# Optimization experiments

Measured on AMD Instinct MI355X. Metric: run time of the kernel, lower is better.

The kernel has to match this reference:

```python
import jax, jax.numpy as jnp
import numpy as np

B, S, D_IN = 2, 2048, 1024
H = 16
HD = 64  # head_dim = d_out // head_cnt


def setup_inputs() -> dict:
    key = jax.random.key(0)
    kx, kq, kk, kv = jax.random.split(key, 4)
    x = jax.random.normal(kx, (B, S, D_IN), dtype=jnp.float32)
    # Per-head Q/K/V projection weights, stacked: [H, d_in, head_dim].
    # Matches nn.Linear(d_in, head_out) per head (qkv_bias=False), scaled like
    # a typical init.
    sc = 1.0 / np.sqrt(D_IN)
    Wq = jax.random.normal(kq, (H, D_IN, HD), dtype=jnp.float32) * sc
    Wk = jax.random.normal(kk, (H, D_IN, HD), dtype=jnp.float32) * sc
    Wv = jax.random.normal(kv, (H, D_IN, HD), dtype=jnp.float32) * sc
    return {"x": x, "Wq": Wq, "Wk": Wk, "Wv": Wv}


def reference(x, Wq, Wk, Wv):
    # Batched multi-head causal attention equivalent to the per-head loop +
    # torch.cat(dim=-1): head h's output occupies slice [h*HD:(h+1)*HD].
    q = jnp.einsum("bsd,hde->bhse", x, Wq)  # [B,H,S,HD]
    k = jnp.einsum("bsd,hde->bhse", x, Wk)
    v = jnp.einsum("bsd,hde->bhse", x, Wv)
    scale = 1.0 / jnp.sqrt(jnp.asarray(HD, dtype=x.dtype))
    scores = jnp.einsum("bhse,bhte->bhst", q, k) * scale  # [B,H,S,S]
    seq = x.shape[1]
    causal = jnp.tril(jnp.ones((seq, seq), dtype=bool))
    scores = jnp.where(causal, scores, jnp.asarray(-jnp.inf, dtype=scores.dtype))
    attn = jax.nn.softmax(scores, axis=-1)  # dropout = 0.0 -> identity
    ctx = jnp.einsum("bhst,bhte->bhse", attn, v)  # [B,H,S,HD]
    # concat heads on last dim
    b, h, s, e = ctx.shape
    return ctx.transpose(0, 2, 1, 3).reshape(b, s, h * e)
```

## Files before the change

### kernel.cpp

```cpp
#include <hip/hip_runtime.h>


#define DI   1024
#define HD   64
#define NH   16
#define SEQ  2048
#define NB   2

typedef unsigned short u16;
typedef unsigned short us8 __attribute__((ext_vector_type(8)));
typedef unsigned short us4 __attribute__((ext_vector_type(4)));
typedef unsigned int   u32x2 __attribute__((ext_vector_type(2)));
typedef short bf8 __attribute__((ext_vector_type(8)));
typedef float f4 __attribute__((ext_vector_type(4)));

#define MFMA16(a, b, c) __builtin_amdgcn_mfma_f32_16x16x32_bf16((a), (b), (c), 0, 0, 0)

#if __has_builtin(__builtin_amdgcn_exp2f)
#define EXP2(x) __builtin_amdgcn_exp2f(x)
#else
#define EXP2(x) exp2f(x)
#endif

#if __has_builtin(__builtin_amdgcn_perm)
#define PKHI(a, b) __builtin_amdgcn_perm((a), (b), 0x07060302u)
#else
__device__ __forceinline__ unsigned PKHI(unsigned a, unsigned b) {
  return (b >> 16) | (a & 0xffff0000u);
}
#endif

__device__ __forceinline__ u16 f2bf(float f) {
  unsigned u = __float_as_uint(f);
  u += 0x7fffu + ((u >> 16) & 1u);
  return (u16)(u >> 16);
}

__device__ __forceinline__ void async16(const u16* g, u16* l) {
  __builtin_amdgcn_global_load_lds((const __attribute__((address_space(1))) void*)g,
                                   (__attribute__((address_space(3))) void*)l,
                                   16, 0, 0);
}

__global__ __launch_bounds__(256) void prep_k(const float* __restrict__ x,
                                              const float* __restrict__ Wq,
                                              const float* __restrict__ Wk,
                                              const float* __restrict__ Wv,
                                              u16* __restrict__ xb,
                                              u16* __restrict__ Wt) {
  __shared__ __align__(16) u16 tile[64][72];
  const int bid = blockIdx.x;
  if (bid < 2048) {
    const int i = (bid * 256 + threadIdx.x) * 8;
    float4 v0 = *(const float4*)(x + i);
    float4 v1 = *(const float4*)(x + i + 4);
    us8 o;
    o[0] = f2bf(v0.x); o[1] = f2bf(v0.y); o[2] = f2bf(v0.z); o[3] = f2bf(v0.w);
    o[4] = f2bf(v1.x); o[5] = f2bf(v1.y); o[6] = f2bf(v1.z); o[7] = f2bf(v1.w);
    *(us8*)(xb + i) = o;
    return;
  }
  const int idx = bid - 2048;
  const int mh = idx >> 4;
  const int d0 = (idx & 15) * 64;
  const int mat = mh >> 4, h = mh & 15;
  const float* W = (mat == 0 ? Wq : (mat == 1 ? Wk : Wv)) + (size_t)h * DI * HD;
  const int t = threadIdx.x;
  {
    const int r = t >> 2, c = (t & 3) * 16;
    const float* src = W + (size_t)(d0 + r) * HD + c;
    #pragma unroll
    for (int j = 0; j < 4; j++) {
      float4 v = *(const float4*)(src + j * 4);
      tile[r][c + j * 4 + 0] = f2bf(v.x);
      tile[r][c + j * 4 + 1] = f2bf(v.y);
      tile[r][c + j * 4 + 2] = f2bf(v.z);
      tile[r][c + j * 4 + 3] = f2bf(v.w);
    }
  }
  __syncthreads();
  {
    const int e = t >> 2, c = (t & 3) * 16;
    __align__(16) u16 tmp[16];
    #pragma unroll
    for (int i = 0; i < 16; i++) tmp[i] = tile[c + i][e];
    u16* dst = Wt + ((size_t)mh * HD + e) * DI + d0 + c;
    *(us8*)dst       = *(us8*)&tmp[0];
    *(us8*)(dst + 8) = *(us8*)&tmp[8];
  }
}

__global__ __launch_bounds__(256, 2) void proj_k(const u16* __restrict__ x,
                                                 const u16* __restrict__ Wt,
                                                 u16* __restrict__ Qo,
                                                 u16* __restrict__ Ko,
                                                 u16* __restrict__ Vo) {
  __shared__ __align__(16) u16 smem[40960];
  u16* const xs = smem;
  u16* const ws = smem + 16384;
  const int m0 = blockIdx.x * 128, n0 = blockIdx.y * 192;
  const int tid = threadIdx.x, w = tid >> 6, lane = tid & 63;
  const int l15 = lane & 15, quad = lane >> 4, l7 = l15 & 7;
  const int lrow = lane >> 3, lch = lane & 7;
  const int wm = w >> 1, wn = w & 1;

  f4 acc[4][6];
  #pragma unroll
  for (int i = 0; i < 4; i++)
    #pragma unroll
    for (int j = 0; j < 6; j++) {
      f4 z = {0.f, 0.f, 0.f, 0.f};
      acc[i][j] = z;
    }

  const u16* xg = x  + (size_t)(m0 + lrow) * DI + ((lch ^ lrow) * 8);
  const u16* wg = Wt + (size_t)(n0 + lrow) * DI + ((lch ^ lrow) * 8);

  #pragma unroll
  for (int i = 0; i < 4; i++)
    async16(xg + (size_t)(i * 32 + w * 8) * DI, &xs[(i * 32 + w * 8) * 64]);
  #pragma unroll
  for (int c = 0; c < 6; c++)
    async16(wg + (size_t)(w * 48 + c * 8) * DI, &ws[(w * 48 + c * 8) * 64]);

  for (int it = 0; it < 16; it++) {
    const int cbx = (it & 1) * 8192, cbw = (it & 1) * 12288;
    __syncthreads();
    if (it + 1 < 16) {
      const int k1 = (it + 1) * 64;
      const int nbx = 8192 - cbx, nbw = 12288 - cbw;
      #pragma unroll
      for (int i = 0; i < 4; i++)
        async16(xg + (size_t)(i * 32 + w * 8) * DI + k1,
                &xs[nbx + (i * 32 + w * 8) * 64]);
      #pragma unroll
      for (int c = 0; c < 6; c++)
        async16(wg + (size_t)(w * 48 + c * 8) * DI + k1,
                &ws[nbw + (w * 48 + c * 8) * 64]);
    }
    #pragma unroll
    for (int ks = 0; ks < 64; ks += 32) {
      const int c0 = (ks >> 3) + quad;
      bf8 af[4], bfr[6];
      #pragma unroll
      for (int i = 0; i < 4; i++)
        af[i] = *(const bf8*)&xs[cbx + (wm * 64 + i * 16 + l15) * 64 + ((c0 ^ l7) * 8)];
      #pragma unroll
      for (int i = 0; i < 6; i++)
        bfr[i] = *(const bf8*)&ws[cbw + (wn * 96 + i * 16 + l15) * 64 + ((c0 ^ l7) * 8)];
      #pragma unroll
      for (int mi = 0; mi < 4; mi++)
        #pragma unroll
        for (int ni = 0; ni < 6; ni++)
          acc[mi][ni] = MFMA16(af[mi], bfr[ni], acc[mi][ni]);
    }
  }

  const float qscale = 0.125f * 1.44269504088896340736f;
  #pragma unroll
  for (int mi = 0; mi < 4; mi++) {
    const int mrow = m0 + wm * 64 + mi * 16 + quad * 4;
    const int b = mrow >> 11, sb = mrow & (SEQ - 1);
    #pragma unroll
    for (int ni = 0; ni < 6; ni++) {
      const int nf = n0 + wn * 96 + ni * 16;
      const int mat = nf >> 10;
      const int h = (nf >> 6) & 15;
      const int e = (nf & 63) + l15;
      if (mat == 2) {
        __align__(8) u16 pk[4];
        #pragma unroll
        for (int r = 0; r < 4; r++) pk[r] = f2bf(acc[mi][ni][r]);
        *(us4*)(Vo + (((size_t)b * NH + h) * HD + e) * SEQ + sb) = *(us4*)pk;
      } else {
        u16* O = mat ? Ko : Qo;
        const float sc = mat ? 1.0f : qscale;
        #pragma unroll
        for (int r = 0; r < 4; r++)
          O[(((size_t)b * NH + h) * SEQ + sb + r) * HD + e] = f2bf(acc[mi][ni][r] * sc);
      }
    }
  }
}

__global__ __launch_bounds__(256, 2) void attn_k(const u16* __restrict__ Qo,
                                                 const u16* __restrict__ Ko,
                                                 const u16* __restrict__ Vo,
                                                 float* __restrict__ out) {
  __shared__ __align__(16) u16 Ks[2 * 128 * 64];
  __shared__ __align__(16) u16 Vs[2 * 64 * 128];
  __shared__ __align__(16) u16 Ps[4 * 16 * 128];
  const int ia = blockIdx.x;
  const int ib = 31 - ia;
  const int bh = blockIdx.y;
  const int b = bh >> 4, h = bh & 15;
  const int tid = threadIdx.x, w = tid >> 6, lane = tid & 63;
  const int l15 = lane & 15, quad = lane >> 4;
  const int qh = quad >> 1, ql = quad & 1;

  const u16* Qb = Qo + (size_t)bh * SEQ * HD;
  const u16* Kb = Ko + (size_t)bh * SEQ * HD;
  const u16* Vb = Vo + (size_t)bh * HD * SEQ;

  const int qrowA = ia * 64 + w * 16 + l15;
  const int qrowB = ib * 64 + w * 16 + l15;
  bf8 bqA0 = *(const bf8*)(Qb + (size_t)qrowA * HD + quad * 8);
  bf8 bqA1 = *(const bf8*)(Qb + (size_t)qrowA * HD + 32 + quad * 8);
  bf8 bqB0 = *(const bf8*)(Qb + (size_t)qrowB * HD + quad * 8);
  bf8 bqB1 = *(const bf8*)(Qb + (size_t)qrowB * HD + 32 + quad * 8);

  f4 oA[4], oB[4], lA, lB;
  #pragma unroll
  for (int i = 0; i < 4; i++) {
    f4 z = {0.f, 0.f, 0.f, 0.f};
    oA[i] = z; oB[i] = z;
  }
  {
    f4 z = {0.f, 0.f, 0.f, 0.f};
    lA = z; lB = z;
  }
  const bf8 ones = {0x3F80, 0x3F80, 0x3F80, 0x3F80, 0x3F80, 0x3F80, 0x3F80, 0x3F80};

  const int nA = ia / 2 + 1, nB = ib / 2 + 1;

  const u16* ksp0 = &Ks[l15 * 64 + ((quad ^ (l15 & 7)) * 8)];
  const u16* ksp1 = &Ks[l15 * 64 + (((quad + 4) ^ (l15 & 7)) * 8)];
  const u16* vsp[4];
  #pragma unroll
  for (int tc = 0; tc < 4; tc++)
    vsp[tc] = &Vs[l15 * 128 + (((tc * 4 + quad) ^ l15) * 8)];
  u16* const psw = &Ps[w * 2048 + l15 * 128 + ql * 4];
  const u16* prp[4];
  #pragma unroll
  for (int tc = 0; tc < 4; tc++)
    prp[tc] = &Ps[w * 2048 + l15 * 128 + (((tc * 4 + quad) ^ l15) * 8)];

  const int kl = lane >> 3, kc = lane & 7;
  const int vl = lane >> 4, vc = lane & 15;
  const u16* kg = Kb + (size_t)(w * 32 + kl) * HD + ((kc ^ kl) * 8);
  const u16* vg[4];
  u16* ldsK[4];
  u16* ldsV[4];
  #pragma unroll
  for (int i = 0; i < 4; i++) {
    const int vr = w * 16 + i * 4;
    const int f = (i * 4 + vl) & 15;
    vg[i] = Vb + (size_t)(vr + vl) * SEQ + ((vc ^ f) * 8);
    ldsK[i] = &Ks[(w * 32 + i * 8) * 64];
    ldsV[i] = &Vs[vr * 128];
  }

  const int mqA = qrowA - (nA - 1) * 128 - quad * 4;
  const int mqB = qrowB - (nB - 1) * 128 - quad * 4;

  auto pphase = [&](f4* s, bool domask, int mq) {
    #pragma unroll
    for (int mf = 0; mf < 8; mf++) {
      f4 sv = s[mf];
      if (domask) {
        #pragma unroll
        for (int r = 0; r < 4; r++)
          sv[r] = (mf * 16 + r <= mq) ? sv[r] : -1e30f;
      }
      const unsigned p0 = __float_as_uint(EXP2(sv[0]));
      const unsigned p1 = __float_as_uint(EXP2(sv[1]));
      const unsigned p2 = __float_as_uint(EXP2(sv[2]));
      const unsigned p3 = __float_as_uint(EXP2(sv[3]));
      u32x2 pk = {PKHI(p1, p0), PKHI(p3, p2)};
      *(u32x2*)(psw + ((((mf << 1) | qh) ^ l15) * 8)) = pk;
    }
  };

  #pragma unroll
  for (int i = 0; i < 4; i++) {
    async16(kg + i * 512, ldsK[i]);
    async16(vg[i], ldsV[i]);
  }
  kg += 128 * HD;
  #pragma unroll
  for (int i = 0; i < 4; i++) vg[i] += 128;

  for (int it = 0; it < nB; it++) {
    const int cb = (it & 1) * 8192;
    __syncthreads();
    if (it + 1 < nB) {
      const int nb = 8192 - cb;
      #pragma unroll
      for (int i = 0; i < 4; i++) {
        async16(kg + i * 512, ldsK[i] + nb);
        async16(vg[i], ldsV[i] + nb);
      }
      kg += 128 * HD;
      #pragma unroll
      for (int i = 0; i < 4; i++) vg[i] += 128;
    }
    const bool doA = (it < nA);

    f4 sA[8], sB[8];
    #pragma unroll
    for (int mf = 0; mf < 8; mf++) {
      bf8 ak0 = *(const bf8*)(ksp0 + cb + mf * 1024);
      bf8 ak1 = *(const bf8*)(ksp1 + cb + mf * 1024);
      f4 z = {0.f, 0.f, 0.f, 0.f};
      f4 tb = MFMA16(ak0, bqB0, z);
      sB[mf] = MFMA16(ak1, bqB1, tb);
      if (doA) {
        f4 ta = MFMA16(ak0, bqA0, z);
        sA[mf] = MFMA16(ak1, bqA1, ta);
      }
    }

    pphase(sB, it == nB - 1, mqB);
    #pragma unroll
    for (int tc = 0; tc < 4; tc++) {
      bf8 pf = *(const bf8*)(prp[tc]);
      lB = MFMA16(ones, pf, lB);
      #pragma unroll
      for (int ef = 0; ef < 4; ef++) {
        bf8 vf = *(const bf8*)(vsp[tc] + cb + ef * 2048);
        oB[ef] = MFMA16(vf, pf, oB[ef]);
      }
    }
    if (doA) {
      pphase(sA, it == nA - 1, mqA);
      #pragma unroll
      for (int tc = 0; tc < 4; tc++) {
        bf8 pf = *(const bf8*)(prp[tc]);
        lA = MFMA16(ones, pf, lA);
        #pragma unroll
        for (int ef = 0; ef < 4; ef++) {
          bf8 vf = *(const bf8*)(vsp[tc] + cb + ef * 2048);
          oA[ef] = MFMA16(vf, pf, oA[ef]);
        }
      }
    }
  }

  const float invA = 1.0f / lA[0];
  const float invB = 1.0f / lB[0];
  float* opA = out + ((size_t)b * SEQ + qrowA) * (NH * HD) + h * HD + quad * 4;
  float* opB = out + ((size_t)b * SEQ + qrowB) * (NH * HD) + h * HD + quad * 4;
  #pragma unroll
  for (int ef = 0; ef < 4; ef++) {
    f4 va = oA[ef] * invA;
    f4 vb = oB[ef] * invB;
    *(float4*)(opA + ef * 16) = *(float4*)&va;
    *(float4*)(opB + ef * 16) = *(float4*)&vb;
  }
}

extern "C" void kernel_launch(void* const* d_in, const int* in_sizes, int n_in,
                              void* d_out, int out_size, void* d_ws, size_t ws_size,
                              hipStream_t stream) {
  const float* x  = (const float*)d_in[0];
  const float* Wq = (const float*)d_in[1];
  const float* Wk = (const float*)d_in[2];
  const float* Wv = (const float*)d_in[3];
  float* out = (float*)d_out;

  u16* xb = (u16*)d_ws;
  u16* Wt = xb + (size_t)NB * SEQ * DI;
  u16* Qo = Wt + (size_t)3 * NH * HD * DI;
  u16* Ko = Qo + (size_t)NB * NH * SEQ * HD;
  u16* Vo = Ko + (size_t)NB * NH * SEQ * HD;

  prep_k<<<dim3(2048 + 768), 256, 0, stream>>>(x, Wq, Wk, Wv, xb, Wt);
  proj_k<<<dim3(32, 16), 256, 0, stream>>>(xb, Wt, Qo, Ko, Vo);
  attn_k<<<dim3(16, 32), 256, 0, stream>>>(Qo, Ko, Vo, out);
}
```

Before: 147.1 us.

## Switch attention to 32x32 MFMA with register-resident P and one 128-row tile per block

Each block now processes a single 128-row query tile with 32x32x16 bf16 MFMAs instead of two paired 64-row tiles using 16x16 MFMAs. The softmax probabilities no longer go through LDS: they are packed and moved between lanes with v_permlane32_swap. The row sums are accumulated in VALU rather than with a ones-matrix MFMA. The work order is reversed for half of the batch-heads to balance causal work, and s_setprio is raised around the MFMA sections. This is meant to cut LDS traffic and MFMA instruction count, at the cost of more registers per thread and coarser load balancing across blocks.

```diff
diff --git a/kernel.cpp b/kernel.cpp
--- a/kernel.cpp
+++ b/kernel.cpp
@@ -13,8 +13,10 @@
 typedef unsigned int   u32x2 __attribute__((ext_vector_type(2)));
 typedef short bf8 __attribute__((ext_vector_type(8)));
 typedef float f4 __attribute__((ext_vector_type(4)));
+typedef float f16v __attribute__((ext_vector_type(16)));
 
 #define MFMA16(a, b, c) __builtin_amdgcn_mfma_f32_16x16x32_bf16((a), (b), (c), 0, 0, 0)
+#define MFMA32(a, b, c) __builtin_amdgcn_mfma_f32_32x32x16_bf16((a), (b), (c), 0, 0, 0)
 
 #if __has_builtin(__builtin_amdgcn_exp2f)
 #define EXP2(x) __builtin_amdgcn_exp2f(x)
@@ -189,51 +191,28 @@
                                                  float* __restrict__ out) {
   __shared__ __align__(16) u16 Ks[2 * 128 * 64];
   __shared__ __align__(16) u16 Vs[2 * 64 * 128];
-  __shared__ __align__(16) u16 Ps[4 * 16 * 128];
-  const int ia = blockIdx.x;
-  const int ib = 31 - ia;
-  const int bh = blockIdx.y;
+  __shared__ float Ls[128];
+  const int xt = blockIdx.x, bh = blockIdx.y;
+  const int t = (bh < 16) ? (15 - xt) : xt;
   const int b = bh >> 4, h = bh & 15;
   const int tid = threadIdx.x, w = tid >> 6, lane = tid & 63;
-  const int l15 = lane & 15, quad = lane >> 4;
-  const int qh = quad >> 1, ql = quad & 1;
+  const int l31 = lane & 31, hi = lane >> 5;
+  const int k7 = l31 & 7, v15 = l31 & 15;
+  const int nI = t + 1;
 
   const u16* Qb = Qo + (size_t)bh * SEQ * HD;
   const u16* Kb = Ko + (size_t)bh * SEQ * HD;
   const u16* Vb = Vo + (size_t)bh * HD * SEQ;
 
-  const int qrowA = ia * 64 + w * 16 + l15;
-  const int qrowB = ib * 64 + w * 16 + l15;
-  bf8 bqA0 = *(const bf8*)(Qb + (size_t)qrowA * HD + quad * 8);
-  bf8 bqA1 = *(const bf8*)(Qb + (size_t)qrowA * HD + 32 + quad * 8);
-  bf8 bqB0 = *(const bf8*)(Qb + (size_t)qrowB * HD + quad * 8);
-  bf8 bqB1 = *(const bf8*)(Qb + (size_t)qrowB * HD + 32 + quad * 8);
-
-  f4 oA[4], oB[4], lA, lB;
-  #pragma unroll
-  for (int i = 0; i < 4; i++) {
-    f4 z = {0.f, 0.f, 0.f, 0.f};
-    oA[i] = z; oB[i] = z;
-  }
-  {
-    f4 z = {0.f, 0.f, 0.f, 0.f};
-    lA = z; lB = z;
-  }
-  const bf8 ones = {0x3F80, 0x3F80, 0x3F80, 0x3F80, 0x3F80, 0x3F80, 0x3F80, 0x3F80};
-
-  const int nA = ia / 2 + 1, nB = ib / 2 + 1;
-
-  const u16* ksp0 = &Ks[l15 * 64 + ((quad ^ (l15 & 7)) * 8)];
-  const u16* ksp1 = &Ks[l15 * 64 + (((quad + 4) ^ (l15 & 7)) * 8)];
-  const u16* vsp[4];
-  #pragma unroll
-  for (int tc = 0; tc < 4; tc++)
-    vsp[tc] = &Vs[l15 * 128 + (((tc * 4 + quad) ^ l15) * 8)];
-  u16* const psw = &Ps[w * 2048 + l15 * 128 + ql * 4];
-  const u16* prp[4];
-  #pragma unroll
-  for (int tc = 0; tc < 4; tc++)
-    prp[tc] = &Ps[w * 2048 + l15 * 128 + (((tc * 4 + quad) ^ l15) * 8)];
+  bf8 bq[4];
+  #pragma unroll
+  for (int ks = 0; ks < 4; ks++)
+    bq[ks] = *(const bf8*)(Qb + (size_t)(t * 128 + w * 32 + l31) * HD + ks * 16 + hi * 8);
+
+  f16v o0, o1, zf;
+  #pragma unroll
+  for (int i = 0; i < 16; i++) { o0[i] = 0.f; o1[i] = 0.f; zf[i] = 0.f; }
+  float lsum = 0.f;
 
   const int kl = lane >> 3, kc = lane & 7;
   const int vl = lane >> 4, vc = lane & 15;
@@ -250,27 +229,6 @@
     ldsV[i] = &Vs[vr * 128];
   }
 
-  const int mqA = qrowA - (nA - 1) * 128 - quad * 4;
-  const int mqB = qrowB - (nB - 1) * 128 - quad * 4;
-
-  auto pphase = [&](f4* s, bool domask, int mq) {
-    #pragma unroll
-    for (int mf = 0; mf < 8; mf++) {
-      f4 sv = s[mf];
-      if (domask) {
-        #pragma unroll
-        for (int r = 0; r < 4; r++)
-          sv[r] = (mf * 16 + r <= mq) ? sv[r] : -1e30f;
-      }
-      const unsigned p0 = __float_as_uint(EXP2(sv[0]));
-      const unsigned p1 = __float_as_uint(EXP2(sv[1]));
-      const unsigned p2 = __float_as_uint(EXP2(sv[2]));
-      const unsigned p3 = __float_as_uint(EXP2(sv[3]));
-      u32x2 pk = {PKHI(p1, p0), PKHI(p3, p2)};
-      *(u32x2*)(psw + ((((mf << 1) | qh) ^ l15) * 8)) = pk;
-    }
-  };
-
   #pragma unroll
   for (int i = 0; i < 4; i++) {
     async16(kg + i * 512, ldsK[i]);
@@ -280,10 +238,12 @@
   #pragma unroll
   for (int i = 0; i < 4; i++) vg[i] += 128;
 
-  for (int it = 0; it < nB; it++) {
+  const int mq = w * 32 + l31;
+
+  for (int it = 0; it < nI; ++it) {
     const int cb = (it & 1) * 8192;
     __syncthreads();
-    if (it + 1 < nB) {
+    if (it + 1 < nI) {
       const int nb = 8192 - cb;
       #pragma unroll
       for (int i = 0; i < 4; i++) {
@@ -294,58 +254,78 @@
       #pragma unroll
       for (int i = 0; i < 4; i++) vg[i] += 128;
     }
-    const bool doA = (it < nA);
-
-    f4 sA[8], sB[8];
-    #pragma unroll
-    for (int mf = 0; mf < 8; mf++) {
-      bf8 ak0 = *(const bf8*)(ksp0 + cb + mf * 1024);
-      bf8 ak1 = *(const bf8*)(ksp1 + cb + mf * 1024);
-      f4 z = {0.f, 0.f, 0.f, 0.f};
-      f4 tb = MFMA16(ak0, bqB0, z);
-      sB[mf] = MFMA16(ak1, bqB1, tb);
-      if (doA) {
-        f4 ta = MFMA16(ak0, bqA0, z);
-        sA[mf] = MFMA16(ak1, bqA1, ta);
-      }
-    }
-
-    pphase(sB, it == nB - 1, mqB);
-    #pragma unroll
-    for (int tc = 0; tc < 4; tc++) {
-      bf8 pf = *(const bf8*)(prp[tc]);
-      lB = MFMA16(ones, pf, lB);
-      #pragma unroll
-      for (int ef = 0; ef < 4; ef++) {
-        bf8 vf = *(const bf8*)(vsp[tc] + cb + ef * 2048);
-        oB[ef] = MFMA16(vf, pf, oB[ef]);
-      }
-    }
-    if (doA) {
-      pphase(sA, it == nA - 1, mqA);
-      #pragma unroll
-      for (int tc = 0; tc < 4; tc++) {
-        bf8 pf = *(const bf8*)(prp[tc]);
-        lA = MFMA16(ones, pf, lA);
-        #pragma unroll
-        for (int ef = 0; ef < 4; ef++) {
-          bf8 vf = *(const bf8*)(vsp[tc] + cb + ef * 2048);
-          oA[ef] = MFMA16(vf, pf, oA[ef]);
+    const bool domask = (it == nI - 1);
+
+    #pragma unroll
+    for (int mf = 0; mf < 4; mf++) {
+      f16v s;
+      __builtin_amdgcn_s_setprio(1);
+      {
+        bf8 ak = *(const bf8*)&Ks[cb + mf * 2048 + l31 * 64 + (((2 * 0 + hi) ^ k7) * 8)];
+        s = MFMA32(ak, bq[0], zf);
+      }
+      #pragma unroll
+      for (int ks = 1; ks < 4; ks++) {
+        bf8 ak = *(const bf8*)&Ks[cb + mf * 2048 + l31 * 64 + (((2 * ks + hi) ^ k7) * 8)];
+        s = MFMA32(ak, bq[ks], s);
+      }
+      __builtin_amdgcn_s_setprio(0);
+
+      unsigned pu[16];
+      #pragma unroll
+      for (int r = 0; r < 16; r++) {
+        float p = EXP2(s[r]);
+        if (domask) {
+          const int kt = mf * 32 + (r & 3) + 8 * (r >> 2) + 4 * hi;
+          p = (kt <= mq) ? p : 0.f;
         }
-      }
-    }
-  }
-
-  const float invA = 1.0f / lA[0];
-  const float invB = 1.0f / lB[0];
-  float* opA = out + ((size_t)b * SEQ + qrowA) * (NH * HD) + h * HD + quad * 4;
-  float* opB = out + ((size_t)b * SEQ + qrowB) * (NH * HD) + h * HD + quad * 4;
-  #pragma unroll
-  for (int ef = 0; ef < 4; ef++) {
-    f4 va = oA[ef] * invA;
-    f4 vb = oB[ef] * invB;
-    *(float4*)(opA + ef * 16) = *(float4*)&va;
-    *(float4*)(opB + ef * 16) = *(float4*)&vb;
+        lsum += p;
+        pu[r] = __float_as_uint(p);
+      }
+      unsigned a0 = PKHI(pu[1],  pu[0]),  a1 = PKHI(pu[3],  pu[2]);
+      unsigned a2 = PKHI(pu[5],  pu[4]),  a3 = PKHI(pu[7],  pu[6]);
+      unsigned a4 = PKHI(pu[9],  pu[8]),  a5 = PKHI(pu[11], pu[10]);
+      unsigned a6 = PKHI(pu[13], pu[12]), a7 = PKHI(pu[15], pu[14]);
+      asm("v_permlane32_swap_b32 %0, %1" : "+v"(a0), "+v"(a2));
+      asm("v_permlane32_swap_b32 %0, %1" : "+v"(a1), "+v"(a3));
+      asm("v_permlane32_swap_b32 %0, %1" : "+v"(a4), "+v"(a6));
+      asm("v_permlane32_swap_b32 %0, %1" : "+v"(a5), "+v"(a7));
+      bf8 pf0, pf1;
+      ((unsigned*)&pf0)[0] = a0; ((unsigned*)&pf0)[1] = a1;
+      ((unsigned*)&pf0)[2] = a2; ((unsigned*)&pf0)[3] = a3;
+      ((unsigned*)&pf1)[0] = a4; ((unsigned*)&pf1)[1] = a5;
+      ((unsigned*)&pf1)[2] = a6; ((unsigned*)&pf1)[3] = a7;
+
+      __builtin_amdgcn_s_setprio(1);
+      {
+        const int c0 = ((4 * mf + hi) ^ v15) * 8;
+        bf8 vf0 = *(const bf8*)&Vs[cb + l31 * 128 + c0];
+        bf8 vf1 = *(const bf8*)&Vs[cb + 4096 + l31 * 128 + c0];
+        o0 = MFMA32(pf0, vf0, o0);
+        o1 = MFMA32(pf0, vf1, o1);
+      }
+      {
+        const int c1 = ((4 * mf + 2 + hi) ^ v15) * 8;
+        bf8 vf0 = *(const bf8*)&Vs[cb + l31 * 128 + c1];
+        bf8 vf1 = *(const bf8*)&Vs[cb + 4096 + l31 * 128 + c1];
+        o0 = MFMA32(pf1, vf0, o0);
+        o1 = MFMA32(pf1, vf1, o1);
+      }
+      __builtin_amdgcn_s_setprio(0);
+    }
+  }
+
+  const float lt = lsum + __shfl_xor(lsum, 32, 64);
+  if (hi == 0) Ls[w * 32 + l31] = lt;
+  __syncthreads();
+
+  float* op = out + ((size_t)(b * SEQ + t * 128 + w * 32)) * (NH * HD) + h * HD + l31;
+  #pragma unroll
+  for (int r = 0; r < 16; r++) {
+    const int qr = (r & 3) + 8 * (r >> 2) + 4 * hi;
+    const float linv = 1.0f / Ls[w * 32 + qr];
+    op[(size_t)qr * (NH * HD)]      = o0[r] * linv;
+    op[(size_t)qr * (NH * HD) + 32] = o1[r] * linv;
   }
 }
 
```

After: 142.5 us. 3.1% less time.
